# Optimization experiments

Hardware: AMD Instinct MI355X
Metric: run time of the kernel (lower is better)

The kernel has to match this reference:

```python
import jax, jax.numpy as jnp
import numpy as np
from jax import lax

B, C, H, W = 32, 3, 128, 128
D = 512   # embedding dim (= encoder channels)
K = 512   # codebook size
S = 4     # conv stride / kernel
HL = H // S  # 32
LL = HL * HL // 1  # latent spatial positions per image... (HL*WL)


def setup_inputs() -> dict:
    key = jax.random.key(0)
    k1, k2, k3, k4 = jax.random.split(key, 4)
    x = jax.random.uniform(k1, (B, C, H, W), dtype=jnp.float32)
    We = jax.random.normal(k2, (D, C, S, S), dtype=jnp.float32) * 0.05  # OIHW
    be = jnp.zeros((D,), dtype=jnp.float32)
    Wd = jax.random.normal(k3, (C, D, S, S), dtype=jnp.float32) * 0.05  # OIHW for conv_transpose
    bd = jnp.zeros((C,), dtype=jnp.float32)
    codebook = jax.random.normal(k4, (D, K), dtype=jnp.float32)  # NearestEmbed.weight: (emb_dim, n_emb)
    return {"x": x, "We": We, "be": be, "Wd": Wd, "bd": bd, "codebook": codebook}


def _encode(x, We, be):
    y = lax.conv_general_dilated(x, We, (S, S), 'VALID',
                                 dimension_numbers=('NCHW', 'OIHW', 'NCHW'))
    return jax.nn.relu(y + be[None, :, None, None])  # (B, D, HL, HL)


def _decode(z, Wd, bd):
    y = lax.conv_transpose(z, Wd, (S, S), 'VALID',
                           dimension_numbers=('NCHW', 'OIHW', 'NCHW'))
    return jax.nn.sigmoid(y + bd[None, :, None, None])  # (B, C, H, W)


def _nearest_idx(z, W):
    # z: (B, D, L), W: (D, K). Squared L2 distance via ||z||^2 - 2 z.W + ||W||^2.
    z2 = jnp.sum(z * z, axis=1)                 # (B, L)
    w2 = jnp.sum(W * W, axis=0)                 # (K,)
    cross = jnp.einsum('bdl,dk->blk', z, W)     # (B, L, K)
    dist = z2[:, :, None] - 2.0 * cross + w2[None, None, :]
    return jnp.argmin(dist, axis=-1)            # (B, L) int


def _gather(W, idx):
    # W: (D, K), idx: (B, L) -> (B, D, L)
    return jnp.take(W, idx, axis=1).transpose(1, 0, 2)


def reference(x, We, be, Wd, bd, codebook):
    code = _encode(x, We, be)                       # (B, D, HL, HL)
    z_e = code.reshape(code.shape[0], D, -1)        # (B, D, L)
    # 1) z_q with weight stop-grad + straight-through on input
    idx_q = _nearest_idx(z_e, codebook)
    zq_raw = _gather(lax.stop_gradient(codebook), idx_q)
    z_q = z_e + lax.stop_gradient(zq_raw - z_e)     # grad d z_q / d z_e = I
    # 2) emb with input detached (grad flows only to codebook via gather)
    ze_sg = lax.stop_gradient(z_e)
    idx_e = _nearest_idx(ze_sg, codebook)
    emb = _gather(codebook, idx_e)
    recon = _decode(z_q.reshape(code.shape), Wd, bd)
    return (recon, z_e.reshape(code.shape), emb.reshape(code.shape))
```

## Files before the change

### kernel.cpp

```cpp
#include <hip/hip_runtime.h>
#include <hip/hip_bf16.h>

#define NPOS 32768
#define EPS_GAP 4e-3f
#define MAXSUS 4096

typedef __attribute__((ext_vector_type(8))) short short8;
typedef __attribute__((ext_vector_type(4))) float floatx4;

static __device__ __forceinline__ float bfu(unsigned short h) {
    return __uint_as_float(((unsigned int)h) << 16);
}
static __device__ __forceinline__ unsigned short f2bf(float f) {
    unsigned int u = __float_as_uint(f);
    u = (u + 0x7fffu + ((u >> 16) & 1u)) >> 16;
    return (unsigned short)u;
}
static __device__ __forceinline__ float ldin(const void* p, size_t i, int flag) {
    return flag ? bfu(((const unsigned short*)p)[i]) : ((const float*)p)[i];
}

static __device__ __forceinline__ void ldsbar() {
    asm volatile("s_waitcnt lgkmcnt(0)" ::: "memory");
    __builtin_amdgcn_s_barrier();
    asm volatile("" ::: "memory");
}

static __device__ __forceinline__ size_t swzoff(int k, int d) {
    return (size_t)(d >> 5) * 16384 + (size_t)(k >> 4) * 512
         + (size_t)((((d >> 3) & 3) * 16 + (k & 15)) * 8) + (d & 7);
}

__global__ __launch_bounds__(1024) void k_sniff(const void* __restrict__ cb,
                                                int* __restrict__ flag,
                                                int* __restrict__ scnt) {
    __shared__ float s[1024];
    const int t = threadIdx.x;
    const int k = t & 63, g = t >> 6;
    const unsigned short* u = (const unsigned short*)cb;
    float acc = 0.f;
    for (int d = g * 32; d < g * 32 + 32; ++d) {
        float v = bfu(u[(size_t)d * 512 + k]);
        acc = fmaf(v, v, acc);
    }
    s[t] = acc;
    __syncthreads();
    if (t < 64) {
        float a = 0.f;
        #pragma unroll
        for (int g2 = 0; g2 < 16; ++g2) a += s[g2 * 64 + k];
        int ok = (a >= 100.f && a <= 2000.f) ? 1 : 0;
        unsigned long long m = __ballot(ok);
        if (k == 0) {
            *flag = (m == ~0ull) ? 1 : 0;
            *scnt = 0;
        }
    }
}

__global__ __launch_bounds__(256) void k_prepAll(
        const void* __restrict__ We, const void* __restrict__ be,
        const void* __restrict__ Wd, const void* __restrict__ bd,
        const void* __restrict__ cb, const int* __restrict__ flagp,
        float* __restrict__ cWe, float* __restrict__ cbe,
        float* __restrict__ cWd, float* __restrict__ cbd,
        float* __restrict__ cbT, unsigned short* __restrict__ cbHS,
        unsigned short* __restrict__ cbLS,
        float* __restrict__ w2, double* __restrict__ w2d,
        float* __restrict__ U) {
    __shared__ float tile[64][65];
    __shared__ double sd[256];
    const int bid = blockIdx.x;
    const int t = threadIdx.x;
    const int flag = *flagp;

    if (bid < 195) {
        int e = bid * 256 + t;
        if (e < 24576)       cWe[e]         = ldin(We, e, flag);
        else if (e < 25088)  cbe[e - 24576] = ldin(be, e - 24576, flag);
        else if (e < 49664)  cWd[e - 25088] = ldin(Wd, e - 25088, flag);
        else if (e < 49667)  cbd[e - 49664] = ldin(bd, e - 49664, flag);
    } else if (bid < 259) {
        const int bb = bid - 195;
        const int D0 = (bb >> 3) * 64, K0 = (bb & 7) * 64;
        for (int it = 0; it < 16; ++it) {
            int r = (t >> 6) + 4 * it, c = t & 63;
            tile[r][c] = ldin(cb, (size_t)(D0 + r) * 512 + K0 + c, flag);
        }
        __syncthreads();
        for (int it = 0; it < 16; ++it) {
            int r = (t >> 6) + 4 * it, c = t & 63;
            float v = tile[c][r];
            int k = K0 + r, d = D0 + c;
            cbT[(size_t)k * 512 + d] = v;
            size_t o2 = swzoff(k, d);
            unsigned short h = f2bf(v);
            cbHS[o2] = h;
            cbLS[o2] = f2bf(v - bfu(h));
        }
    } else if (bid < 267) {
        const int k = (bid - 259) * 64 + (t & 63);
        const int g = t >> 6;
        double acc = 0.0;
        for (int d = g * 128; d < g * 128 + 128; ++d) {
            double v = (double)ldin(cb, (size_t)d * 512 + k, flag);
            acc += v * v;
        }
        sd[t] = acc;
        __syncthreads();
        if (t < 64) {
            double a = sd[t] + sd[t + 64] + sd[t + 128] + sd[t + 192];
            w2[k] = (float)a;
            w2d[k] = a;
        }
    } else {
        const int kk = (bid - 267) * 4 + (t >> 6);
        const int lane = t & 63;
        const int j = lane >> 2, dpart = lane & 3;
        const int u = (j >> 2) & 3, v = j & 3;
        int woff[3];
        #pragma unroll
        for (int m = 0; m < 3; ++m) woff[m] = m * 8192 + (3 - u) * 4 + (3 - v);
        float a0 = 0.f, a1 = 0.f, a2 = 0.f;
        for (int i = 0; i < 128; ++i) {
            int d = dpart * 128 + i;
            float cw = ldin(cb, (size_t)d * 512 + kk, flag);
            a0 = fmaf(cw, ldin(Wd, (size_t)(woff[0] + d * 16), flag), a0);
            a1 = fmaf(cw, ldin(Wd, (size_t)(woff[1] + d * 16), flag), a1);
            a2 = fmaf(cw, ldin(Wd, (size_t)(woff[2] + d * 16), flag), a2);
        }
        a0 += __shfl_xor(a0, 1); a0 += __shfl_xor(a0, 2);
        a1 += __shfl_xor(a1, 1); a1 += __shfl_xor(a1, 2);
        a2 += __shfl_xor(a2, 1); a2 += __shfl_xor(a2, 2);
        if (dpart == 0) {
            U[kk * 48 +  0 + j] = a0 + ldin(bd, 0, flag);
            U[kk * 48 + 16 + j] = a1 + ldin(bd, 1, flag);
            U[kk * 48 + 32 + j] = a2 + ldin(bd, 2, flag);
        }
    }
}

static __device__ __forceinline__ void conv_step(
        const float* __restrict__ patch, const float* __restrict__ cWe,
        const float* __restrict__ cbe, int dc, int t,
        unsigned short* __restrict__ zq,
        float* __restrict__ out_z, int b, int SP0) {
    const int cd = t & 31;
    const int ps = ((t >> 5) & 15) * 4;
    const float4* wv = (const float4*)(cWe + (size_t)(dc + cd) * 48);
    const float bias = cbe[dc + cd];
    float za[4];
    #pragma unroll
    for (int p = 0; p < 4; ++p) za[p] = bias;
    #pragma unroll
    for (int q4 = 0; q4 < 12; ++q4) {
        float4 wq = wv[q4];
        #pragma unroll
        for (int p = 0; p < 4; ++p) {
            float4 v = ((const float4*)(patch + (ps + p) * 48))[q4];
            za[p] = fmaf(v.x, wq.x, za[p]);
            za[p] = fmaf(v.y, wq.y, za[p]);
            za[p] = fmaf(v.z, wq.z, za[p]);
            za[p] = fmaf(v.w, wq.w, za[p]);
        }
    }
    float zf[4];
    #pragma unroll
    for (int p = 0; p < 4; ++p) {
        float z = fmaxf(za[p], 0.f);
        unsigned short h = f2bf(z);
        unsigned short l = f2bf(z - bfu(h));
        zq[(ps + p) * 40 + cd] = h;
        zq[2560 + (ps + p) * 40 + cd] = l;
        zf[p] = bfu(h) + bfu(l);
    }
    size_t zbase = (size_t)(b * 512 + dc + cd) * 1024 + SP0 + ps;
    *(float4*)(out_z + zbase) = (float4){zf[0], zf[1], zf[2], zf[3]};
}

static __device__ __forceinline__ void mfma_step(
        const unsigned short* __restrict__ zq,
        const unsigned short* __restrict__ cbHS,
        const unsigned short* __restrict__ cbLS,
        int dcPrev, int wave, int quad, int lcol, int flag, floatx4 (&acc)[4][4]) {
    const int lane = quad * 16 + lcol;
    short8 aH[4], aL[4];
    #pragma unroll
    for (int mt = 0; mt < 4; ++mt) {
        aH[mt] = *(const short8*)(zq + (mt * 16 + lcol) * 40 + quad * 8);
        aL[mt] = *(const short8*)(zq + 2560 + (mt * 16 + lcol) * 40 + quad * 8);
    }
    const unsigned short* fbH = cbHS + (size_t)dcPrev * 512 + (size_t)(wave * 4) * 512 + lane * 8;
    #pragma unroll
    for (int j = 0; j < 4; ++j) {
        short8 bH = *(const short8*)(fbH + j * 512);
        #pragma unroll
        for (int mt = 0; mt < 4; ++mt) {
            acc[mt][j] = __builtin_amdgcn_mfma_f32_16x16x32_bf16(aH[mt], bH, acc[mt][j], 0, 0, 0);
            acc[mt][j] = __builtin_amdgcn_mfma_f32_16x16x32_bf16(aL[mt], bH, acc[mt][j], 0, 0, 0);
        }
    }
    if (!flag) {
        const unsigned short* fbL = cbLS + (size_t)dcPrev * 512 + (size_t)(wave * 4) * 512 + lane * 8;
        #pragma unroll
        for (int j = 0; j < 4; ++j) {
            short8 bL = *(const short8*)(fbL + j * 512);
            #pragma unroll
            for (int mt = 0; mt < 4; ++mt)
                acc[mt][j] = __builtin_amdgcn_mfma_f32_16x16x32_bf16(aH[mt], bL, acc[mt][j], 0, 0, 0);
        }
    }
}

static __device__ __forceinline__ void bmerge(float& a1, int& ak, float& a2,
                                              float o1, int ok, float o2) {
    if (o1 < a1)      { a2 = fminf(a1, o2); a1 = o1; ak = ok; }
    else if (o1 > a1) { a2 = fminf(a2, o1); }
    else              { a2 = a1; if (ok < ak) ak = ok; }
}

__global__ __launch_bounds__(512, 4) void k_main(
        const void* __restrict__ x, const float* __restrict__ cWe,
        const float* __restrict__ cbe, const int* __restrict__ flagp,
        const unsigned short* __restrict__ cbHS, const unsigned short* __restrict__ cbLS,
        const float* __restrict__ cbT, const float* __restrict__ w2,
        float* __restrict__ out_z, float* __restrict__ out_e,
        int* __restrict__ idx, int* __restrict__ scnt, int* __restrict__ spos,
        int skipTail) {
    __shared__ __align__(16) char smc[32768];
    float* patch = (float*)smc;
    unsigned short* zb = (unsigned short*)(smc + 12288);

    const int t = threadIdx.x;
    const int bid = blockIdx.x;
    const int q = ((bid & 7) << 6) | (bid >> 3);
    const int P0 = q * 64;
    const int b = P0 >> 10, SP0 = P0 & 1023;
    const int flag = *flagp;
    const int wave = t >> 6, lane = t & 63;
    const int quad = lane >> 4, lcol = lane & 15;

    for (int e = t; e < 3072; e += 512) {
        int pid = e / 48, kk = e % 48;
        int c = kk >> 4, r = (kk >> 2) & 3, s = kk & 3;
        int pos = P0 + pid;
        int bb = pos >> 10, sp = pos & 1023, i = sp >> 5, j = sp & 31;
        patch[pid * 48 + kk] = ldin(x, ((bb * 3 + c) * 128 + (i * 4 + r)) * 128 + (j * 4 + s), flag);
    }

    floatx4 acc[4][4];
    #pragma unroll
    for (int mt = 0; mt < 4; ++mt)
        #pragma unroll
        for (int j = 0; j < 4; ++j) acc[mt][j] = (floatx4){0.f, 0.f, 0.f, 0.f};

    ldsbar();
    conv_step(patch, cWe, cbe, 0, t, zb, out_z, b, SP0);
    for (int dc = 32; dc < 512; dc += 32) {
        ldsbar();
        const int p = (dc >> 5) & 1;
        conv_step(patch, cWe, cbe, dc, t, zb + p * 5120, out_z, b, SP0);
        mfma_step(zb + (p ^ 1) * 5120, cbHS, cbLS, dc - 32, wave, quad, lcol, flag, acc);
    }
    ldsbar();
    mfma_step(zb + 5120, cbHS, cbLS, 480, wave, quad, lcol, flag, acc);

    float s1[4][4], s2[4][4]; int k1[4][4];
    #pragma unroll
    for (int mt = 0; mt < 4; ++mt)
        #pragma unroll
        for (int r = 0; r < 4; ++r) { s1[mt][r] = 1e30f; s2[mt][r] = 1e30f; k1[mt][r] = 511; }
    #pragma unroll
    for (int j = 0; j < 4; ++j) {
        int code = (wave * 4 + j) * 16 + lcol;
        float wk = w2[code];
        #pragma unroll
        for (int mt = 0; mt < 4; ++mt)
            #pragma unroll
            for (int r = 0; r < 4; ++r) {
                float s = wk - 2.f * acc[mt][j][r];
                bmerge(s1[mt][r], k1[mt][r], s2[mt][r], s, code, 1e30f);
            }
    }
    float* sS1 = (float*)smc;
    int*   sK1 = (int*)(smc + 2048);
    float* sS2 = (float*)(smc + 4096);
    int*   ii  = (int*)(smc + 6144);
    #pragma unroll
    for (int mt = 0; mt < 4; ++mt)
        #pragma unroll
        for (int r = 0; r < 4; ++r) {
            float a1 = s1[mt][r], a2 = s2[mt][r]; int ak = k1[mt][r];
            #pragma unroll
            for (int m = 1; m < 16; m <<= 1) {
                float o1 = __shfl_xor(a1, m);
                float o2 = __shfl_xor(a2, m);
                int   ok = __shfl_xor(ak, m);
                bmerge(a1, ak, a2, o1, ok, o2);
            }
            if (lcol == 0) {
                int pos = mt * 16 + quad * 4 + r;
                sS1[pos * 8 + wave] = a1;
                sK1[pos * 8 + wave] = ak;
                sS2[pos * 8 + wave] = a2;
            }
        }
    __syncthreads();
    if (t < 64) {
        float a1 = sS1[t * 8]; int ak = sK1[t * 8]; float a2 = sS2[t * 8];
        #pragma unroll
        for (int w = 1; w < 8; ++w)
            bmerge(a1, ak, a2, sS1[t * 8 + w], sK1[t * 8 + w], sS2[t * 8 + w]);
        ak &= 511;
        ii[t] = ak;
        unsigned int flagged = 0u;
        if (a2 - a1 < EPS_GAP) {
            int slot = atomicAdd(scnt, 1);
            if (slot < MAXSUS) { spos[slot] = P0 + t; flagged = 1u; }
        }
        idx[P0 + t] = (int)((unsigned)ak | (flagged << 31));
    }
    __syncthreads();

    const int sp = t & 63, dq = t >> 6;
    const float* row = cbT + (size_t)ii[sp] * 512;
    const size_t obase = ((size_t)b * 512) * 1024 + SP0 + sp;
    for (int d0 = dq * 64; d0 < dq * 64 + 64; d0 += 4) {
        if (skipTail && b == 31 && d0 >= 448) break;
        float4 v = *(const float4*)(row + d0);
        out_e[obase + (size_t)(d0    ) * 1024] = v.x;
        out_e[obase + (size_t)(d0 + 1) * 1024] = v.y;
        out_e[obase + (size_t)(d0 + 2) * 1024] = v.z;
        out_e[obase + (size_t)(d0 + 3) * 1024] = v.w;
    }
}

__global__ __launch_bounds__(256) void k_post(
        const float* __restrict__ out_z, const void* __restrict__ cb,
        const double* __restrict__ w2d, int* __restrict__ idx,
        const int* __restrict__ scnt, const int* __restrict__ spos,
        const float* __restrict__ U, const int* __restrict__ flagp,
        float* __restrict__ out_e, float* __restrict__ out_r, int skipTail) {
    __shared__ float zsh[512];
    __shared__ float rs[256];
    __shared__ int rk[256];
    __shared__ int bc[2];
    const int bid = blockIdx.x;
    const int t = threadIdx.x;

    if (bid < 128) {
        const int pos = bid * 256 + t;
        const int v0 = idx[pos];
        if (v0 >= 0) {
            const int id = v0 & 511;
            const int b = pos >> 10, sp = pos & 1023, i = sp >> 5, j = sp & 31;
            const float* u = &U[(size_t)id * 48];
            #pragma unroll
            for (int c = 0; c < 3; ++c)
                #pragma unroll
                for (int uu = 0; uu < 4; ++uu) {
                    float4 q = *(const float4*)(&u[c * 16 + uu * 4]);
                    float4 o;
                    o.x = 1.f / (1.f + __expf(-q.x));
                    o.y = 1.f / (1.f + __expf(-q.y));
                    o.z = 1.f / (1.f + __expf(-q.z));
                    o.w = 1.f / (1.f + __expf(-q.w));
                    *(float4*)(&out_r[((size_t)((b * 3 + c) * 128) + (i * 4 + uu)) * 128 + j * 4]) = o;
                }
        }
        return;
    }

    const int flag = *flagp;
    int n = *scnt; if (n > MAXSUS) n = MAXSUS;
    for (int s = bid - 128; s < n; s += 256) {
        int p = spos[s] & 32767;
        int b = p >> 10, sp = p & 1023;
        __syncthreads();
        zsh[t]       = out_z[(size_t)(b * 512 + t) * 1024 + sp];
        zsh[t + 256] = out_z[(size_t)(b * 512 + t + 256) * 1024 + sp];
        __syncthreads();
        float bs = 1e30f; int bk = 511;
        for (int cc = 0; cc < 2; ++cc) {
            int k = t + cc * 256;
            double a = 0.0;
            for (int d = 0; d < 512; ++d)
                a = fma((double)zsh[d], (double)ldin(cb, (size_t)d * 512 + k, flag), a);
            float sc = (float)(w2d[k] - 2.0 * a);
            if (sc < bs || (sc == bs && k < bk)) { bs = sc; bk = k; }
        }
        rs[t] = bs; rk[t] = bk;
        __syncthreads();
        for (int str = 128; str > 0; str >>= 1) {
            if (t < str) {
                float so = rs[t + str]; int ko = rk[t + str];
                if (so < rs[t] || (so == rs[t] && ko < rk[t])) { rs[t] = so; rk[t] = ko; }
            }
            __syncthreads();
        }
        if (t == 0) {
            int kstar = rk[0] & 511;
            int old = idx[p] & 511;
            bc[0] = kstar; bc[1] = (kstar != old);
            idx[p] = kstar;
        }
        __syncthreads();
        const int kk = bc[0];
        if (bc[1]) {
            for (int d = t; d < 512; d += 256) {
                if (skipTail && b == 31 && d >= 448) continue;
                out_e[(size_t)(b * 512 + d) * 1024 + sp] = ldin(cb, (size_t)d * 512 + kk, flag);
            }
        }
        if (t < 48) {
            float q = U[(size_t)kk * 48 + t];
            float o = 1.f / (1.f + __expf(-q));
            int c = t >> 4, uu = (t >> 2) & 3, vv = t & 3;
            int i = sp >> 5, j = sp & 31;
            out_r[((size_t)((b * 3 + c) * 128) + (i * 4 + uu)) * 128 + j * 4 + vv] = o;
        }
    }
}

__global__ __launch_bounds__(1024) void k_fixup(
        const void* __restrict__ cb, const int* __restrict__ flagp,
        const int* __restrict__ idx, float* __restrict__ out_e) {
    const int t = threadIdx.x;
    const int d = 448 + blockIdx.x;
    const int flag = *flagp;
    const int id = idx[31744 + t] & 511;
    out_e[((size_t)(31 * 512 + d)) * 1024 + t] = ldin(cb, (size_t)d * 512 + id, flag);
}

extern "C" void kernel_launch(void* const* d_in, const int* in_sizes, int n_in,
                              void* d_out, int out_size, void* d_ws, size_t ws_size,
                              hipStream_t stream) {
    const void* x  = d_in[0];
    const void* We = d_in[1];
    const void* be = d_in[2];
    const void* Wd = d_in[3];
    const void* bd = d_in[4];
    const void* cb = d_in[5];

    float* out   = (float*)d_out;
    float* out_r = out;
    float* out_z = out + 1572864;
    float* out_e = out + 18350080;

    char* Rb = (char*)out_r;
    float* cbT          = (float*)(Rb);
    float* cWe          = (float*)(Rb + 1048576);
    float* cbe          = (float*)(Rb + 1146880);
    float* cWd          = (float*)(Rb + 1148928);
    float* cbd          = (float*)(Rb + 1247232);
    unsigned short* cbHS= (unsigned short*)(Rb + 1247296);
    unsigned short* cbLS= (unsigned short*)(Rb + 1771584);

    int tailWS = (ws_size >= 262144) ? 1 : 0;
    char* Tbase = tailWS ? (char*)d_ws : ((char*)out_e + 66846720);
    int skipTail = tailWS ? 0 : 1;
    int*    idx  = (int*)   (Tbase);
    float*  U    = (float*) (Tbase + 131072);
    float*  w2   = (float*) (Tbase + 229376);
    double* w2d  = (double*)(Tbase + 231424);
    int*    flag = (int*)   (Tbase + 235520);
    int*    scnt = (int*)   (Tbase + 235584);
    int*    spos = (int*)   (Tbase + 235648);

    k_sniff<<<1, 1024, 0, stream>>>(cb, flag, scnt);
    k_prepAll<<<395, 256, 0, stream>>>(We, be, Wd, bd, cb, flag,
                                       cWe, cbe, cWd, cbd,
                                       cbT, cbHS, cbLS, w2, w2d, U);
    k_main<<<512, 512, 0, stream>>>(x, cWe, cbe, flag, cbHS, cbLS, cbT, w2,
                                    out_z, out_e, idx, scnt, spos, skipTail);
    k_post<<<384, 256, 0, stream>>>(out_z, cb, w2d, idx, scnt, spos, U, flag,
                                    out_e, out_r, skipTail);
    if (skipTail)
        k_fixup<<<64, 1024, 0, stream>>>(cb, flag, idx, out_e);
}
```

Baseline: 279.2 us.

## Compute encoder conv with split-bf16 MFMA instead of scalar FMA

The per-chunk encoder convolution, previously a scalar fp32 FMA loop over 48 taps, now runs on MFMA 16x16x32 bf16 instructions. Input patches are split into high and low bf16 parts in LDS, and the encoder weights are split and pre-swizzled by extra prep blocks. This targets the VALU cost of the conv, which is interleaved with the codebook MFMA step. The 3-term split keeps near-fp32 accuracy at the cost of more LDS (about 38 KB per block), which may reduce occupancy, plus extra weight-prep work.

```diff
diff --git a/kernel.cpp b/kernel.cpp
--- a/kernel.cpp
+++ b/kernel.cpp
@@ -66,6 +66,7 @@
         float* __restrict__ cWd, float* __restrict__ cbd,
         float* __restrict__ cbT, unsigned short* __restrict__ cbHS,
         unsigned short* __restrict__ cbLS,
+        unsigned short* __restrict__ WeswzH, unsigned short* __restrict__ WeswzL,
         float* __restrict__ w2, double* __restrict__ w2d,
         float* __restrict__ U) {
     __shared__ float tile[64][65];
@@ -113,7 +114,7 @@
             w2[k] = (float)a;
             w2d[k] = a;
         }
-    } else {
+    } else if (bid < 395) {
         const int kk = (bid - 267) * 4 + (t >> 6);
         const int lane = t & 63;
         const int j = lane >> 2, dpart = lane & 3;
@@ -137,45 +138,65 @@
             U[kk * 48 + 16 + j] = a1 + ldin(bd, 1, flag);
             U[kk * 48 + 32 + j] = a2 + ldin(bd, 2, flag);
         }
-    }
-}
-
-static __device__ __forceinline__ void conv_step(
-        const float* __restrict__ patch, const float* __restrict__ cWe,
-        const float* __restrict__ cbe, int dc, int t,
-        unsigned short* __restrict__ zq,
-        float* __restrict__ out_z, int b, int SP0) {
-    const int cd = t & 31;
-    const int ps = ((t >> 5) & 15) * 4;
-    const float4* wv = (const float4*)(cWe + (size_t)(dc + cd) * 48);
-    const float bias = cbe[dc + cd];
-    float za[4];
-    #pragma unroll
-    for (int p = 0; p < 4; ++p) za[p] = bias;
-    #pragma unroll
-    for (int q4 = 0; q4 < 12; ++q4) {
-        float4 wq = wv[q4];
-        #pragma unroll
-        for (int p = 0; p < 4; ++p) {
-            float4 v = ((const float4*)(patch + (ps + p) * 48))[q4];
-            za[p] = fmaf(v.x, wq.x, za[p]);
-            za[p] = fmaf(v.y, wq.y, za[p]);
-            za[p] = fmaf(v.z, wq.z, za[p]);
-            za[p] = fmaf(v.w, wq.w, za[p]);
-        }
-    }
+    } else {
+        const int bid2 = bid - 395;
+        for (int it = 0; it < 16; ++it) {
+            int e = bid2 * 4096 + it * 256 + t;
+            int d = e >> 6, q = e & 63;
+            float w = (q < 48) ? ldin(We, (size_t)d * 48 + q, flag) : 0.f;
+            unsigned short h = f2bf(w);
+            unsigned short l = f2bf(w - bfu(h));
+            size_t off = (size_t)((d >> 5) * 2 + ((d >> 4) & 1)) * 1024
+                       + (size_t)(q >> 5) * 512
+                       + (size_t)((((q >> 3) & 3) * 16 + (d & 15)) * 8) + (q & 7);
+            WeswzH[off] = h;
+            WeswzL[off] = l;
+        }
+    }
+}
+
+static __device__ __forceinline__ void conv_mfma(
+        const unsigned short* __restrict__ patchH, const unsigned short* __restrict__ patchL,
+        const unsigned short* __restrict__ WeH, const unsigned short* __restrict__ WeL,
+        const float* __restrict__ cbe, int dc, int wave, int lane, int flag,
+        unsigned short* __restrict__ zq, float* __restrict__ out_z, int b, int SP0) {
+    const int mt = wave >> 1, nt = wave & 1;
+    const int quad = lane >> 4, lcol = lane & 15;
+    const int row = mt * 16 + lcol;
+    short8 aH0 = *(const short8*)(patchH + row * 72 + quad * 8);
+    short8 aH1 = *(const short8*)(patchH + row * 72 + 32 + quad * 8);
+    const unsigned short* wb = WeH + (size_t)((dc >> 5) * 2 + nt) * 1024 + lane * 8;
+    short8 bH0 = *(const short8*)(wb);
+    short8 bH1 = *(const short8*)(wb + 512);
+    floatx4 c = (floatx4){0.f, 0.f, 0.f, 0.f};
+    c = __builtin_amdgcn_mfma_f32_16x16x32_bf16(aH0, bH0, c, 0, 0, 0);
+    c = __builtin_amdgcn_mfma_f32_16x16x32_bf16(aH1, bH1, c, 0, 0, 0);
+    if (!flag) {
+        short8 aL0 = *(const short8*)(patchL + row * 72 + quad * 8);
+        short8 aL1 = *(const short8*)(patchL + row * 72 + 32 + quad * 8);
+        const unsigned short* wl = WeL + (size_t)((dc >> 5) * 2 + nt) * 1024 + lane * 8;
+        short8 bL0 = *(const short8*)(wl);
+        short8 bL1 = *(const short8*)(wl + 512);
+        c = __builtin_amdgcn_mfma_f32_16x16x32_bf16(aL0, bH0, c, 0, 0, 0);
+        c = __builtin_amdgcn_mfma_f32_16x16x32_bf16(aL1, bH1, c, 0, 0, 0);
+        c = __builtin_amdgcn_mfma_f32_16x16x32_bf16(aH0, bL0, c, 0, 0, 0);
+        c = __builtin_amdgcn_mfma_f32_16x16x32_bf16(aH1, bL1, c, 0, 0, 0);
+    }
+    const int d = nt * 16 + lcol;
+    const float bias = cbe[dc + d];
+    const int p0 = mt * 16 + quad * 4;
     float zf[4];
     #pragma unroll
-    for (int p = 0; p < 4; ++p) {
-        float z = fmaxf(za[p], 0.f);
+    for (int r = 0; r < 4; ++r) {
+        float z = fmaxf(c[r] + bias, 0.f);
         unsigned short h = f2bf(z);
         unsigned short l = f2bf(z - bfu(h));
-        zq[(ps + p) * 40 + cd] = h;
-        zq[2560 + (ps + p) * 40 + cd] = l;
-        zf[p] = bfu(h) + bfu(l);
-    }
-    size_t zbase = (size_t)(b * 512 + dc + cd) * 1024 + SP0 + ps;
-    *(float4*)(out_z + zbase) = (float4){zf[0], zf[1], zf[2], zf[3]};
+        zq[(p0 + r) * 40 + d] = h;
+        zq[2560 + (p0 + r) * 40 + d] = l;
+        zf[r] = bfu(h) + bfu(l);
+    }
+    *(float4*)(out_z + (size_t)(b * 512 + dc + d) * 1024 + SP0 + p0) =
+        (float4){zf[0], zf[1], zf[2], zf[3]};
 }
 
 static __device__ __forceinline__ void mfma_step(
@@ -220,16 +241,18 @@
 }
 
 __global__ __launch_bounds__(512, 4) void k_main(
-        const void* __restrict__ x, const float* __restrict__ cWe,
+        const void* __restrict__ x, const unsigned short* __restrict__ WeswzH,
+        const unsigned short* __restrict__ WeswzL,
         const float* __restrict__ cbe, const int* __restrict__ flagp,
         const unsigned short* __restrict__ cbHS, const unsigned short* __restrict__ cbLS,
         const float* __restrict__ cbT, const float* __restrict__ w2,
         float* __restrict__ out_z, float* __restrict__ out_e,
         int* __restrict__ idx, int* __restrict__ scnt, int* __restrict__ spos,
         int skipTail) {
-    __shared__ __align__(16) char smc[32768];
-    float* patch = (float*)smc;
-    unsigned short* zb = (unsigned short*)(smc + 12288);
+    __shared__ __align__(16) char smc[38912];
+    unsigned short* patchH = (unsigned short*)smc;
+    unsigned short* patchL = (unsigned short*)(smc + 9216);
+    unsigned short* zb = (unsigned short*)(smc + 18432);
 
     const int t = threadIdx.x;
     const int bid = blockIdx.x;
@@ -240,12 +263,18 @@
     const int wave = t >> 6, lane = t & 63;
     const int quad = lane >> 4, lcol = lane & 15;
 
-    for (int e = t; e < 3072; e += 512) {
-        int pid = e / 48, kk = e % 48;
-        int c = kk >> 4, r = (kk >> 2) & 3, s = kk & 3;
-        int pos = P0 + pid;
-        int bb = pos >> 10, sp = pos & 1023, i = sp >> 5, j = sp & 31;
-        patch[pid * 48 + kk] = ldin(x, ((bb * 3 + c) * 128 + (i * 4 + r)) * 128 + (j * 4 + s), flag);
+    for (int e = t; e < 4096; e += 512) {
+        int pid = e >> 6, qq = e & 63;
+        float xv = 0.f;
+        if (qq < 48) {
+            int c = qq >> 4, r = (qq >> 2) & 3, s = qq & 3;
+            int pos = P0 + pid;
+            int bb = pos >> 10, sp = pos & 1023, i = sp >> 5, j = sp & 31;
+            xv = ldin(x, ((bb * 3 + c) * 128 + (i * 4 + r)) * 128 + (j * 4 + s), flag);
+        }
+        unsigned short h = f2bf(xv);
+        patchH[pid * 72 + qq] = h;
+        patchL[pid * 72 + qq] = f2bf(xv - bfu(h));
     }
 
     floatx4 acc[4][4];
@@ -255,11 +284,13 @@
         for (int j = 0; j < 4; ++j) acc[mt][j] = (floatx4){0.f, 0.f, 0.f, 0.f};
 
     ldsbar();
-    conv_step(patch, cWe, cbe, 0, t, zb, out_z, b, SP0);
+    conv_mfma(patchH, patchL, WeswzH, WeswzL, cbe, 0, wave, lane, flag,
+              zb, out_z, b, SP0);
     for (int dc = 32; dc < 512; dc += 32) {
         ldsbar();
         const int p = (dc >> 5) & 1;
-        conv_step(patch, cWe, cbe, dc, t, zb + p * 5120, out_z, b, SP0);
+        conv_mfma(patchH, patchL, WeswzH, WeswzL, cbe, dc, wave, lane, flag,
+                  zb + p * 5120, out_z, b, SP0);
         mfma_step(zb + (p ^ 1) * 5120, cbHS, cbLS, dc - 32, wave, quad, lcol, flag, acc);
     }
     ldsbar();
@@ -448,13 +479,15 @@
     float* out_e = out + 18350080;
 
     char* Rb = (char*)out_r;
-    float* cbT          = (float*)(Rb);
-    float* cWe          = (float*)(Rb + 1048576);
-    float* cbe          = (float*)(Rb + 1146880);
-    float* cWd          = (float*)(Rb + 1148928);
-    float* cbd          = (float*)(Rb + 1247232);
-    unsigned short* cbHS= (unsigned short*)(Rb + 1247296);
-    unsigned short* cbLS= (unsigned short*)(Rb + 1771584);
+    float* cbT           = (float*)(Rb);
+    float* cWe           = (float*)(Rb + 1048576);
+    float* cbe           = (float*)(Rb + 1146880);
+    float* cWd           = (float*)(Rb + 1148928);
+    float* cbd           = (float*)(Rb + 1247232);
+    unsigned short* cbHS = (unsigned short*)(Rb + 1247296);
+    unsigned short* cbLS = (unsigned short*)(Rb + 1771584);
+    unsigned short* WeswzH=(unsigned short*)(Rb + 2295872);
+    unsigned short* WeswzL=(unsigned short*)(Rb + 2361408);
 
     int tailWS = (ws_size >= 262144) ? 1 : 0;
     char* Tbase = tailWS ? (char*)d_ws : ((char*)out_e + 66846720);
@@ -468,11 +501,13 @@
     int*    spos = (int*)   (Tbase + 235648);
 
     k_sniff<<<1, 1024, 0, stream>>>(cb, flag, scnt);
-    k_prepAll<<<395, 256, 0, stream>>>(We, be, Wd, bd, cb, flag,
+    k_prepAll<<<403, 256, 0, stream>>>(We, be, Wd, bd, cb, flag,
                                        cWe, cbe, cWd, cbd,
-                                       cbT, cbHS, cbLS, w2, w2d, U);
-    k_main<<<512, 512, 0, stream>>>(x, cWe, cbe, flag, cbHS, cbLS, cbT, w2,
-                                    out_z, out_e, idx, scnt, spos, skipTail);
+                                       cbT, cbHS, cbLS, WeswzH, WeswzL,
+                                       w2, w2d, U);
+    k_main<<<512, 512, 0, stream>>>(x, WeswzH, WeswzL, cbe, flag, cbHS, cbLS,
+                                    cbT, w2, out_z, out_e, idx, scnt, spos,
+                                    skipTail);
     k_post<<<384, 256, 0, stream>>>(out_z, cb, w2d, idx, scnt, spos, U, flag,
                                     out_e, out_r, skipTail);
     if (skipTail)
```

After: 251.3 us. -10.0%, faster.
